# Kernel tuning notes

Hardware: AMD Instinct MI355X
Metric: run time of the kernel (lower is better)

Reference implementation:

```python
import jax, jax.numpy as jnp
import numpy as np

B, V, F, O = 256, 512, 256, 2


def setup_inputs() -> dict:
    key = jax.random.key(0)
    k1, k2, k3, k4, k5, k6 = jax.random.split(key, 6)
    features = jax.random.normal(k1, (B, V, F), dtype=jnp.float32)
    graphs = jax.random.randint(k2, (B, V, V), 0, 2, dtype=jnp.int32)
    # GCNConv params: lin (no bias) weight [F, O] + separate bias [O]
    conv_weight = jax.random.normal(k3, (F, O), dtype=jnp.float32) / np.sqrt(F)
    conv_bias = jax.random.normal(k4, (O,), dtype=jnp.float32) * 0.01
    # head: Linear(O*V, 1)
    lin_weight = jax.random.normal(k5, (1, O * V), dtype=jnp.float32) / np.sqrt(O * V)
    lin_bias = jax.random.normal(k6, (1,), dtype=jnp.float32) * 0.01
    return {"features": features, "graphs": graphs, "conv_weight": conv_weight,
            "conv_bias": conv_bias, "lin_weight": lin_weight, "lin_bias": lin_bias}


def reference(features, graphs, conv_weight, conv_bias, lin_weight, lin_bias):
    # dense_to_sparse -> binary edges (edge values discarded, weight 1)
    adj = (graphs != 0).astype(features.dtype)  # [B, V, V]
    # gcn_norm: add remaining self-loops (diag = 1), symmetric normalization
    eye = jnp.eye(V, dtype=features.dtype)
    adj = jnp.where(eye > 0, 1.0, adj)
    deg = adj.sum(axis=-1)  # [B, V]
    dinv = jnp.where(deg > 0, jax.lax.rsqrt(jnp.maximum(deg, 1e-30)), 0.0)
    norm_adj = dinv[:, :, None] * adj * dinv[:, None, :]  # D^-1/2 (A+I) D^-1/2
    # GCNConv: aggregate then affine (order commutes): A_hat X W + b
    h = jnp.einsum("bvw,bwf,fo->bvo", norm_adj, features, conv_weight) + conv_bias
    h = jax.nn.relu(h).reshape(B, V * O)  # flatten(start_dim=1) of [B, V, O]
    logits = h @ lin_weight.T + lin_bias  # [B, 1]
    return jax.nn.sigmoid(logits)
```

## Files before the change

kernel.cpp:

```cpp
#include <hip/hip_runtime.h>

#define Bn 256
#define Vn 512
#define Fn 256

#define WS_PACKED_OFF 0
#define WS_DINV_OFF   8388608
#define WS_Y_OFF      8912896

__global__ __launch_bounds__(256) void pack_deg_kernel(
    const int* __restrict__ G,
    unsigned long long* __restrict__ P,
    float* __restrict__ dinv) {
  int gid  = blockIdx.x * 256 + threadIdx.x;
  int row  = gid >> 6;
  int lane = gid & 63;
  int v    = row & (Vn - 1);

  const int* r = G + (size_t)row * Vn;
  int x0 = r[  0 + lane];
  int x1 = r[ 64 + lane];
  int x2 = r[128 + lane];
  int x3 = r[192 + lane];
  int x4 = r[256 + lane];
  int x5 = r[320 + lane];
  int x6 = r[384 + lane];
  int x7 = r[448 + lane];

  unsigned long long m0 = __ballot(x0 != 0);
  unsigned long long m1 = __ballot(x1 != 0);
  unsigned long long m2 = __ballot(x2 != 0);
  unsigned long long m3 = __ballot(x3 != 0);
  unsigned long long m4 = __ballot(x4 != 0);
  unsigned long long m5 = __ballot(x5 != 0);
  unsigned long long m6 = __ballot(x6 != 0);
  unsigned long long m7 = __ballot(x7 != 0);

  int j = v >> 6;
  unsigned long long db = 1ull << (v & 63);
  if (j == 0) m0 |= db;
  else if (j == 1) m1 |= db;
  else if (j == 2) m2 |= db;
  else if (j == 3) m3 |= db;
  else if (j == 4) m4 |= db;
  else if (j == 5) m5 |= db;
  else if (j == 6) m6 |= db;
  else             m7 |= db;

  int deg = __popcll(m0) + __popcll(m1) + __popcll(m2) + __popcll(m3) +
            __popcll(m4) + __popcll(m5) + __popcll(m6) + __popcll(m7);

  unsigned long long sel = m0;
  sel = (lane == 1) ? m1 : sel;
  sel = (lane == 2) ? m2 : sel;
  sel = (lane == 3) ? m3 : sel;
  sel = (lane == 4) ? m4 : sel;
  sel = (lane == 5) ? m5 : sel;
  sel = (lane == 6) ? m6 : sel;
  sel = (lane == 7) ? m7 : sel;
  if (lane < 8) P[(size_t)row * 8 + lane] = sel;
  if (lane == 0) dinv[row] = rsqrtf((float)deg);
}

__global__ __launch_bounds__(256) void xw_kernel(
    const float* __restrict__ X,
    const float* __restrict__ W,
    float2* __restrict__ Y) {
  int gid  = blockIdx.x * 256 + threadIdx.x;
  int row  = gid >> 6;
  int lane = gid & 63;

  const float4* xr = (const float4*)(X + (size_t)row * Fn);
  float4 x = xr[lane];
  const float4* wr = (const float4*)W;
  float4 w0 = wr[lane * 2];
  float4 w1 = wr[lane * 2 + 1];

  float s0 = x.x * w0.x + x.y * w0.z + x.z * w1.x + x.w * w1.z;
  float s1 = x.x * w0.y + x.y * w0.w + x.z * w1.y + x.w * w1.w;
  #pragma unroll
  for (int off = 32; off; off >>= 1) {
    s0 += __shfl_xor(s0, off);
    s1 += __shfl_xor(s1, off);
  }
  if (lane == 0) Y[row] = make_float2(s0, s1);
}

__global__ __launch_bounds__(256) void agg_head_kernel(
    const unsigned long long* __restrict__ P,
    const float* __restrict__ dinv,
    const float2* __restrict__ Y,
    const float* __restrict__ lw,
    const float* __restrict__ lb,
    const float* __restrict__ cb,
    float* __restrict__ out) {
  __shared__ float2 ylds[Vn];
  __shared__ float wsum[4];

  int b = blockIdx.x;
  int t = threadIdx.x;

  #pragma unroll
  for (int i = t; i < Vn; i += 256) {
    float  d = dinv[b * Vn + i];
    float2 y = Y[b * Vn + i];
    ylds[i] = make_float2(y.x * d, y.y * d);
  }
  __syncthreads();

  int v0 = t, v1 = t + 256;
  const unsigned long long* p0 = P + ((size_t)b * Vn + v0) * 8;
  const unsigned long long* p1 = P + ((size_t)b * Vn + v1) * 8;

  float a00 = 0.f, a01 = 0.f, a10 = 0.f, a11 = 0.f;
  for (int j = 0; j < 8; ++j) {
    unsigned long long m0 = p0[j];
    unsigned long long m1 = p1[j];
    const float2* yj = ylds + j * 64;
    #pragma unroll
    for (int k = 0; k < 64; ++k) {
      float2 y = yj[k];
      float s0 = (float)((m0 >> k) & 1ull);
      float s1 = (float)((m1 >> k) & 1ull);
      a00 = fmaf(s0, y.x, a00);
      a01 = fmaf(s0, y.y, a01);
      a10 = fmaf(s1, y.x, a10);
      a11 = fmaf(s1, y.y, a11);
    }
  }

  float d0 = dinv[b * Vn + v0];
  float d1 = dinv[b * Vn + v1];
  float cb0 = cb[0], cb1 = cb[1];
  const float2* lw2 = (const float2*)lw;
  float2 w0v = lw2[v0];
  float2 w1v = lw2[v1];

  float h00 = fmaxf(fmaf(d0, a00, cb0), 0.f);
  float h01 = fmaxf(fmaf(d0, a01, cb1), 0.f);
  float h10 = fmaxf(fmaf(d1, a10, cb0), 0.f);
  float h11 = fmaxf(fmaf(d1, a11, cb1), 0.f);
  float c = h00 * w0v.x + h01 * w0v.y + h10 * w1v.x + h11 * w1v.y;

  #pragma unroll
  for (int off = 32; off; off >>= 1) c += __shfl_xor(c, off);
  if ((t & 63) == 0) wsum[t >> 6] = c;
  __syncthreads();
  if (t == 0) {
    float logit = wsum[0] + wsum[1] + wsum[2] + wsum[3] + lb[0];
    out[b] = 1.0f / (1.0f + expf(-logit));
  }
}

extern "C" void kernel_launch(void* const* d_in, const int* in_sizes, int n_in,
                              void* d_out, int out_size, void* d_ws, size_t ws_size,
                              hipStream_t stream) {
  const float* features = (const float*)d_in[0];
  const int*   graphs   = (const int*)d_in[1];
  const float* conv_w   = (const float*)d_in[2];
  const float* conv_b   = (const float*)d_in[3];
  const float* lin_w    = (const float*)d_in[4];
  const float* lin_b    = (const float*)d_in[5];
  float* out = (float*)d_out;

  char* ws = (char*)d_ws;
  unsigned long long* P = (unsigned long long*)(ws + WS_PACKED_OFF);
  float*  dinv = (float*)(ws + WS_DINV_OFF);
  float2* Y    = (float2*)(ws + WS_Y_OFF);

  pack_deg_kernel<<<dim3(32768), dim3(256), 0, stream>>>(graphs, P, dinv);
  xw_kernel<<<dim3(32768), dim3(256), 0, stream>>>(features, conv_w, Y);
  agg_head_kernel<<<dim3(Bn), dim3(256), 0, stream>>>(P, dinv, Y, lin_w, lin_b, conv_b, out);
}
```

Baseline: 451.2 us.

## Fuse adjacency bit-packing and XW projection into one kernel with int4 loads

Merges the adjacency pack/degree kernel and the feature-times-weight kernel into one launch. Each wave now reads its adjacency row as int4 vectors, which changes the bit layout of the packed masks to an interleaved order; the aggregation kernel is updated to index Y with a stride of 4 to match. This removes one kernel launch and improves load vectorisation on the dominant 134MB adjacency read. The strided LDS access in aggregation may add bank conflicts.

After: 459.8 us. Within noise of the previous version (+1.9%).

```diff
diff --git a/kernel.cpp b/kernel.cpp
--- a/kernel.cpp
+++ b/kernel.cpp
@@ -8,82 +8,62 @@
 #define WS_DINV_OFF   8388608
 #define WS_Y_OFF      8912896
 
-__global__ __launch_bounds__(256) void pack_deg_kernel(
-    const int* __restrict__ G,
+__global__ __launch_bounds__(256) void fused_stage_kernel(
+    const int4* __restrict__ G4,
+    const float* __restrict__ X,
+    const float* __restrict__ W,
     unsigned long long* __restrict__ P,
-    float* __restrict__ dinv) {
+    float* __restrict__ dinv,
+    float2* __restrict__ Y) {
   int gid  = blockIdx.x * 256 + threadIdx.x;
   int row  = gid >> 6;
   int lane = gid & 63;
   int v    = row & (Vn - 1);
 
-  const int* r = G + (size_t)row * Vn;
-  int x0 = r[  0 + lane];
-  int x1 = r[ 64 + lane];
-  int x2 = r[128 + lane];
-  int x3 = r[192 + lane];
-  int x4 = r[256 + lane];
-  int x5 = r[320 + lane];
-  int x6 = r[384 + lane];
-  int x7 = r[448 + lane];
-
-  unsigned long long m0 = __ballot(x0 != 0);
-  unsigned long long m1 = __ballot(x1 != 0);
-  unsigned long long m2 = __ballot(x2 != 0);
-  unsigned long long m3 = __ballot(x3 != 0);
-  unsigned long long m4 = __ballot(x4 != 0);
-  unsigned long long m5 = __ballot(x5 != 0);
-  unsigned long long m6 = __ballot(x6 != 0);
-  unsigned long long m7 = __ballot(x7 != 0);
-
-  int j = v >> 6;
-  unsigned long long db = 1ull << (v & 63);
-  if (j == 0) m0 |= db;
-  else if (j == 1) m1 |= db;
-  else if (j == 2) m2 |= db;
-  else if (j == 3) m3 |= db;
-  else if (j == 4) m4 |= db;
-  else if (j == 5) m5 |= db;
-  else if (j == 6) m6 |= db;
-  else             m7 |= db;
-
-  int deg = __popcll(m0) + __popcll(m1) + __popcll(m2) + __popcll(m3) +
-            __popcll(m4) + __popcll(m5) + __popcll(m6) + __popcll(m7);
-
-  unsigned long long sel = m0;
-  sel = (lane == 1) ? m1 : sel;
-  sel = (lane == 2) ? m2 : sel;
-  sel = (lane == 3) ? m3 : sel;
-  sel = (lane == 4) ? m4 : sel;
-  sel = (lane == 5) ? m5 : sel;
-  sel = (lane == 6) ? m6 : sel;
-  sel = (lane == 7) ? m7 : sel;
-  if (lane < 8) P[(size_t)row * 8 + lane] = sel;
-  if (lane == 0) dinv[row] = rsqrtf((float)deg);
-}
-
-__global__ __launch_bounds__(256) void xw_kernel(
-    const float* __restrict__ X,
-    const float* __restrict__ W,
-    float2* __restrict__ Y) {
-  int gid  = blockIdx.x * 256 + threadIdx.x;
-  int row  = gid >> 6;
-  int lane = gid & 63;
+  const int4* gr = G4 + (size_t)row * (Vn / 4);
+  int4 g0 = gr[lane];
+  int4 g1 = gr[lane + 64];
 
   const float4* xr = (const float4*)(X + (size_t)row * Fn);
-  float4 x = xr[lane];
+  float4 xf = xr[lane];
   const float4* wr = (const float4*)W;
   float4 w0 = wr[lane * 2];
   float4 w1 = wr[lane * 2 + 1];
 
-  float s0 = x.x * w0.x + x.y * w0.z + x.z * w1.x + x.w * w1.z;
-  float s1 = x.x * w0.y + x.y * w0.w + x.z * w1.y + x.w * w1.w;
+  unsigned long long m[8];
+  m[0] = __ballot(g0.x != 0);
+  m[1] = __ballot(g0.y != 0);
+  m[2] = __ballot(g0.z != 0);
+  m[3] = __ballot(g0.w != 0);
+  m[4] = __ballot(g1.x != 0);
+  m[5] = __ballot(g1.y != 0);
+  m[6] = __ballot(g1.z != 0);
+  m[7] = __ballot(g1.w != 0);
+
+  int widx = ((v >> 8) << 2) | (v & 3);
+  unsigned long long db = 1ull << ((v >> 2) & 63);
+  #pragma unroll
+  for (int i = 0; i < 8; ++i) m[i] |= (widx == i) ? db : 0ull;
+
+  int deg = __popcll(m[0]) + __popcll(m[1]) + __popcll(m[2]) + __popcll(m[3]) +
+            __popcll(m[4]) + __popcll(m[5]) + __popcll(m[6]) + __popcll(m[7]);
+
+  float s0 = xf.x * w0.x + xf.y * w0.z + xf.z * w1.x + xf.w * w1.z;
+  float s1 = xf.x * w0.y + xf.y * w0.w + xf.z * w1.y + xf.w * w1.w;
   #pragma unroll
   for (int off = 32; off; off >>= 1) {
     s0 += __shfl_xor(s0, off);
     s1 += __shfl_xor(s1, off);
   }
-  if (lane == 0) Y[row] = make_float2(s0, s1);
+
+  unsigned long long sel = m[0];
+  #pragma unroll
+  for (int i = 1; i < 8; ++i) sel = (lane == i) ? m[i] : sel;
+  if (lane < 8) P[(size_t)row * 8 + lane] = sel;
+  if (lane == 0) {
+    dinv[row] = rsqrtf((float)deg);
+    Y[row] = make_float2(s0, s1);
+  }
 }
 
 __global__ __launch_bounds__(256) void agg_head_kernel(
@@ -113,19 +93,23 @@
   const unsigned long long* p1 = P + ((size_t)b * Vn + v1) * 8;
 
   float a00 = 0.f, a01 = 0.f, a10 = 0.f, a11 = 0.f;
-  for (int j = 0; j < 8; ++j) {
-    unsigned long long m0 = p0[j];
-    unsigned long long m1 = p1[j];
-    const float2* yj = ylds + j * 64;
+  #pragma unroll
+  for (int c = 0; c < 2; ++c) {
     #pragma unroll
-    for (int k = 0; k < 64; ++k) {
-      float2 y = yj[k];
-      float s0 = (float)((m0 >> k) & 1ull);
-      float s1 = (float)((m1 >> k) & 1ull);
-      a00 = fmaf(s0, y.x, a00);
-      a01 = fmaf(s0, y.y, a01);
-      a10 = fmaf(s1, y.x, a10);
-      a11 = fmaf(s1, y.y, a11);
+    for (int j = 0; j < 4; ++j) {
+      unsigned long long m0 = p0[c * 4 + j];
+      unsigned long long m1 = p1[c * 4 + j];
+      const float2* base = ylds + c * 256 + j;
+      #pragma unroll
+      for (int k = 0; k < 64; ++k) {
+        float2 y = base[k * 4];
+        float s0 = (float)((m0 >> k) & 1ull);
+        float s1 = (float)((m1 >> k) & 1ull);
+        a00 = fmaf(s0, y.x, a00);
+        a01 = fmaf(s0, y.y, a01);
+        a10 = fmaf(s1, y.x, a10);
+        a11 = fmaf(s1, y.y, a11);
+      }
     }
   }
 
@@ -168,7 +152,7 @@
   float*  dinv = (float*)(ws + WS_DINV_OFF);
   float2* Y    = (float2*)(ws + WS_Y_OFF);
 
-  pack_deg_kernel<<<dim3(32768), dim3(256), 0, stream>>>(graphs, P, dinv);
-  xw_kernel<<<dim3(32768), dim3(256), 0, stream>>>(features, conv_w, Y);
+  fused_stage_kernel<<<dim3(32768), dim3(256), 0, stream>>>(
+      (const int4*)graphs, features, conv_w, P, dinv, Y);
   agg_head_kernel<<<dim3(Bn), dim3(256), 0, stream>>>(P, dinv, Y, lin_w, lin_b, conv_b, out);
 }
```
